# Kernel optimization log

Measured on AMD Instinct MI355X. Metric: run time of the kernel, lower is better.

The kernel has to match this reference:

```python
import jax, jax.numpy as jnp
import numpy as np

NS = [65536, 16384, 4096, 1024, 256, 64]          # nodes per level (64 = 8 graphs x 8 dense voxels)
ES = [1048576, 262144, 65536, 16384, 4096]        # edges per level (avg degree 16)
INS = [1, 15, 23, 31, 39]
OUTS = [12, 20, 28, 36, 44]
K = 5                                             # kernel_size


def setup_inputs():
    keys = iter(jax.random.split(jax.random.key(0), 64))
    d = {'x': jax.random.normal(next(keys), (NS[0], 1), jnp.float32),
         'pos': jax.random.uniform(next(keys), (NS[0], 3), jnp.float32)}
    for l in range(5):
        n, e, ci, co = NS[l], ES[l], INS[l], OUTS[l]
        d[f'src{l}'] = jax.random.randint(next(keys), (e,), 0, n)
        d[f'dst{l}'] = jax.random.randint(next(keys), (e,), 0, n)
        d[f'eattr{l}'] = jax.random.normal(next(keys), (e, 3), jnp.float32)
        d[f'cluster{l}'] = jax.random.randint(next(keys), (n,), 0, NS[l + 1])
        d[f'w1_{l}'] = jax.random.normal(next(keys), (3, K), jnp.float32) * 0.5
        d[f'b1_{l}'] = jnp.zeros((K,), jnp.float32)
        d[f'w2_{l}'] = jax.random.normal(next(keys), (K, ci * co), jnp.float32) / np.float32(np.sqrt(K * ci))
        d[f'b2_{l}'] = jnp.zeros((ci * co,), jnp.float32)
        d[f'root_{l}'] = jax.random.normal(next(keys), (ci, co), jnp.float32) / np.float32(np.sqrt(ci))
        d[f'bias_{l}'] = jnp.zeros((co,), jnp.float32)
    d['fc_w'] = jax.random.normal(next(keys), (8 * 47, 10), jnp.float32) / np.float32(np.sqrt(8 * 47))
    d['fc_b'] = jnp.zeros((10,), jnp.float32)
    return d


def _conv(x, src, dst, eattr, w1, b1, w2, b2, root, bias, n):
    # edge-conditioned kernel: MLP(edge_attr) -> [E, ci, co]
    h = jnp.tanh(eattr @ w1 + b1)                                  # [E, K]
    We = (h @ w2 + b2).reshape(eattr.shape[0], x.shape[1], -1)     # [E, ci, co]
    msg = jnp.einsum('ei,eio->eo', x[src], We)                     # gather + per-edge matvec
    s = jax.ops.segment_sum(msg, dst, num_segments=n)
    cnt = jax.ops.segment_sum(jnp.ones((dst.shape[0], 1), x.dtype), dst, num_segments=n)
    agg = s / jnp.maximum(cnt, 1.0)                                # mean aggregation
    return agg + x @ root + bias, jnp.mean(jnp.square(We))


def _pool(x, pos, cluster, n_next):
    # sparse voxel max pool on features, mean on positions; pos concatenated to features
    xm = jax.ops.segment_max(x, cluster, num_segments=n_next)
    xm = jnp.where(jnp.isfinite(xm), xm, 0.0)                      # empty voxels -> 0
    ps = jax.ops.segment_sum(pos, cluster, num_segments=n_next)
    cnt = jax.ops.segment_sum(jnp.ones((pos.shape[0], 1), pos.dtype), cluster, num_segments=n_next)
    pm = ps / jnp.maximum(cnt, 1.0)
    return jnp.concatenate([xm, pm], axis=1), pm


def reference(x, pos, src0, dst0, eattr0, cluster0, w1_0, b1_0, w2_0, b2_0, root_0, bias_0,
              src1, dst1, eattr1, cluster1, w1_1, b1_1, w2_1, b2_1, root_1, bias_1,
              src2, dst2, eattr2, cluster2, w1_2, b1_2, w2_2, b2_2, root_2, bias_2,
              src3, dst3, eattr3, cluster3, w1_3, b1_3, w2_3, b2_3, root_3, bias_3,
              src4, dst4, eattr4, cluster4, w1_4, b1_4, w2_4, b2_4, root_4, bias_4,
              fc_w, fc_b):
    lv = [(src0, dst0, eattr0, cluster0, w1_0, b1_0, w2_0, b2_0, root_0, bias_0),
          (src1, dst1, eattr1, cluster1, w1_1, b1_1, w2_1, b2_1, root_1, bias_1),
          (src2, dst2, eattr2, cluster2, w1_2, b1_2, w2_2, b2_2, root_2, bias_2),
          (src3, dst3, eattr3, cluster3, w1_3, b1_3, w2_3, b2_3, root_3, bias_3),
          (src4, dst4, eattr4, cluster4, w1_4, b1_4, w2_4, b2_4, root_4, bias_4)]
    closs = jnp.float32(0.0)
    for l, (src, dst, ea, cl, w1, b1, w2, b2, rt, bs) in enumerate(lv):
        x, c = _conv(x, src, dst, ea, w1, b1, w2, b2, rt, bs, NS[l])
        closs = closs + c
        x, pos = _pool(x, pos, cl, NS[l + 1])
    feat = x.reshape(-1, 8 * 47)                                   # [B, 8*47]
    logits = feat @ fc_w + fc_b
    return jax.nn.log_softmax(logits, axis=1), closs
```

## Files before the change

### kernel.cpp

```cpp
#include <hip/hip_runtime.h>
#include <hip/hip_fp16.h>
#include <math.h>


#define NBUCK 8
#define TILES0 256
#define NB0    512
#define IDXCAP 3072
#define TILES1 64
#define NB1    512

struct SegArgs {
    const int* idx[10];
    int*       cnt[10];
    int*       rp [10];
    int*       out[10];
    int        n  [10];
    int        nb [10];
    int        shift[10];
    int        tstart[11];
};

struct ScanAux {
    int* tilesum;
    int* tileoff;
    int  sstart[11];
    int  T;
};

struct HArgs {
    const float* eattr[5];
    const float* w1[5];
    const float* b1[5];
    float*       H;
    int          E[5];
    int          bstart[6];
};

struct WArgs {
    const float* w2[5];
    const float* b2[5];
    const float* H;
    float*       sq;
    int          cico[5];
    int          E[5];
};

__global__ __launch_bounds__(256) void countA_k(
    SegArgs a, HArgs ha, const int* __restrict__ dst0,
    const int* __restrict__ dst1, int* __restrict__ M, int* __restrict__ M1,
    int histBlocks)
{
    __shared__ int sh[NB0];
    int B = blockIdx.x;
    int t = threadIdx.x;

    if (B < TILES0) {
        for (int u = t; u < NB0; u += 256) sh[u] = 0;
        __syncthreads();
        int base = B * 4096 + t;
        #pragma unroll
        for (int it = 0; it < 16; it++)
            atomicAdd(&sh[dst0[base + it * 256] >> 7], 1);
        __syncthreads();
        for (int u = t; u < NB0; u += 256) M[(size_t)B * NB0 + u] = sh[u];
        return;
    }
    B -= TILES0;
    if (B < TILES1) {
        for (int u = t; u < NB1; u += 256) sh[u] = 0;
        __syncthreads();
        int base = B * 4096 + t;
        #pragma unroll
        for (int it = 0; it < 16; it++)
            atomicAdd(&sh[dst1[base + it * 256] >> 5], 1);
        __syncthreads();
        for (int u = t; u < NB1; u += 256) M1[(size_t)B * NB1 + u] = sh[u];
        return;
    }
    B -= TILES1;
    if (B < histBlocks) {
        int bucket = B % NBUCK;
        int T = B / NBUCK;
        int s = 0;
        while (s < 9 && T >= a.tstart[s + 1]) s++;
        int i = (T - a.tstart[s]) * 256 + t;
        if (i >= a.n[s]) return;
        int d = a.idx[s][i];
        if ((d >> a.shift[s]) != bucket) return;
        atomicAdd(&a.cnt[s][d], 1);
        return;
    }
    int b = B - histBlocks;
    const int K = 32;
    int l = 0;
    while (l < 4 && b >= ha.bstart[l + 1]) l++;
    int bloc = b - ha.bstart[l];
    const float* ea = ha.eattr[l];
    float w1r[15], b1r[5];
    #pragma unroll
    for (int i = 0; i < 15; i++) w1r[i] = ha.w1[l][i];
    #pragma unroll
    for (int i = 0; i < 5; i++)  b1r[i] = ha.b1[l][i];
    float acc[20];
    #pragma unroll
    for (int i = 0; i < 20; i++) acc[i] = 0.f;
    int base = bloc * 256 * K + t;
    for (int it = 0; it < K; it++) {
        int e = base + it * 256;
        if (e < ha.E[l]) {
            float e0 = ea[e * 3], e1 = ea[e * 3 + 1], e2 = ea[e * 3 + 2];
            float h[5];
            #pragma unroll
            for (int k = 0; k < 5; k++)
                h[k] = tanhf(e0 * w1r[k] + e1 * w1r[5 + k] + e2 * w1r[10 + k] + b1r[k]);
            int p = 5;
            #pragma unroll
            for (int k = 0; k < 5; k++) {
                acc[k] += h[k];
                #pragma unroll
                for (int k2 = k; k2 < 5; k2++) acc[p++] += h[k] * h[k2];
            }
        }
    }
    float* red = (float*)sh;
    int wid = t >> 6, lane = t & 63;
    #pragma unroll
    for (int v = 0; v < 20; v++) {
        float s = acc[v];
        #pragma unroll
        for (int o = 32; o; o >>= 1) s += __shfl_down(s, o);
        if (lane == 0) red[wid * 20 + v] = s;
    }
    __syncthreads();
    if (t < 20)
        atomicAdd(&ha.H[l * 20 + t],
                  red[t] + red[20 + t] + red[40 + t] + red[60 + t]);
}

__global__ __launch_bounds__(256) void scanP1_k(
    SegArgs a, ScanAux x, const int* __restrict__ M, int* __restrict__ M2,
    int* __restrict__ colTotal, const int* __restrict__ M1,
    int* __restrict__ M21, int* __restrict__ ct1)
{
    __shared__ int sc[256];
    int B = blockIdx.x;
    int t = threadIdx.x;

    if (B < NB0) {
        int v = M[(size_t)t * NB0 + B];
        sc[t] = v;
        __syncthreads();
        for (int d = 1; d < 256; d <<= 1) {
            int u = (t >= d) ? sc[t - d] : 0;
            __syncthreads();
            sc[t] += u;
            __syncthreads();
        }
        M2[(size_t)t * NB0 + B] = sc[t] - v;
        if (t == 255) colTotal[B] = sc[255];
        return;
    }
    B -= NB0;
    if (B < NB1) {
        if (t >= 64) return;
        int v = M1[(size_t)t * NB1 + B];
        int val = v;
        #pragma unroll
        for (int d = 1; d < 64; d <<= 1) {
            int u = __shfl_up(val, d);
            if (t >= d) val += u;
        }
        M21[(size_t)t * NB1 + B] = val - v;
        if (t == 63) ct1[B] = val;
        return;
    }
    int b = B - NB1;
    int s = 0;
    while (s < 9 && b >= x.sstart[s + 1]) s++;
    int tloc = b - x.sstart[s];
    int nb = a.nb[s];
    const int* cnt = a.cnt[s];
    int i0 = tloc * 4096 + t * 16;
    int sum = 0;
    #pragma unroll
    for (int k = 0; k < 16; k++) {
        int i = i0 + k;
        if (i < nb) sum += cnt[i];
    }
    #pragma unroll
    for (int o = 32; o; o >>= 1) sum += __shfl_down(sum, o);
    if ((t & 63) == 0) sc[t >> 6] = sum;
    __syncthreads();
    if (t == 0)
        x.tilesum[b] = sc[0] + sc[1] + sc[2] + sc[3];
}

__global__ __launch_bounds__(512) void scanP2_k(
    SegArgs a, ScanAux x, const int* __restrict__ colTotal,
    int* __restrict__ bucketStart, const int* __restrict__ ct1,
    int* __restrict__ bs1)
{
    __shared__ int sc[NB0];
    int t = threadIdx.x;
    if (blockIdx.x == 0) {
        int v = colTotal[t];
        sc[t] = v;
        __syncthreads();
        for (int d = 1; d < NB0; d <<= 1) {
            int u = (t >= d) ? sc[t - d] : 0;
            __syncthreads();
            sc[t] += u;
            __syncthreads();
        }
        bucketStart[t] = sc[t] - v;
        if (t == NB0 - 1) bucketStart[NB0] = sc[NB0 - 1];
        return;
    }
    if (blockIdx.x == 2) {
        int v = ct1[t];
        sc[t] = v;
        __syncthreads();
        for (int d = 1; d < NB1; d <<= 1) {
            int u = (t >= d) ? sc[t - d] : 0;
            __syncthreads();
            sc[t] += u;
            __syncthreads();
        }
        bs1[t] = sc[t] - v;
        if (t == NB1 - 1) bs1[NB1] = sc[NB1 - 1];
        return;
    }
    if (t >= 64) return;
    int lane = t;
    int orig = (lane < x.T) ? x.tilesum[lane] : 0;
    int val = orig;
    #pragma unroll
    for (int d = 1; d < 64; d <<= 1) {
        int v = __shfl_up(val, d);
        if (lane >= d) val += v;
    }
    int excl = val - orig;
    int s = 0;
    while (s < 9 && lane >= x.sstart[s + 1]) s++;
    int segExcl = __shfl(excl, x.sstart[s]);
    if (lane < x.T) {
        x.tileoff[lane] = excl - segExcl;
        if (lane == x.sstart[s + 1] - 1)
            a.rp[s][a.nb[s]] = val - segExcl;
    }
}

__global__ __launch_bounds__(256) void scanP3_k(
    SegArgs a, ScanAux x,
    const int* __restrict__ src, const int* __restrict__ dst,
    const float* __restrict__ ea, const float* __restrict__ x0,
    const int* __restrict__ M2, const int* __restrict__ bucketStart,
    float4* __restrict__ pay2,
    const float* __restrict__ w1, const float* __restrict__ b1,
    float* __restrict__ H0,
    const int* __restrict__ src1, const int* __restrict__ dst1,
    const float* __restrict__ ea1, const int* __restrict__ M21,
    const int* __restrict__ bs1, float4* __restrict__ pay1)
{
    __shared__ int   shi[NB0];
    __shared__ float shf[100];
    int B = blockIdx.x;
    int t = threadIdx.x;

    if (B < x.T) {
        int s = 0;
        while (s < 9 && B >= x.sstart[s + 1]) s++;
        int tloc = B - x.sstart[s];
        int nb = a.nb[s];
        const int* cnt = a.cnt[s];
        int* rp = a.rp[s];
        int i0 = tloc * 4096 + t * 16;
        int v[16];
        int sum = 0;
        #pragma unroll
        for (int k = 0; k < 16; k++) {
            int i = i0 + k;
            v[k] = (i < nb) ? cnt[i] : 0;
            sum += v[k];
        }
        int acc = sum;
        shi[t] = acc;
        __syncthreads();
        for (int d = 1; d < 256; d <<= 1) {
            int t2 = (t >= d) ? shi[t - d] : 0;
            __syncthreads();
            acc += t2;
            shi[t] = acc;
            __syncthreads();
        }
        int running = x.tileoff[B] + (acc - sum);
        #pragma unroll
        for (int k = 0; k < 16; k++) {
            int i = i0 + k;
            if (i < nb) rp[i] = running;
            running += v[k];
        }
        return;
    }
    B -= x.T;
    if (B < TILES0) {
        int tile = B;
        for (int u = t; u < NB0; u += 256)
            shi[u] = bucketStart[u] + M2[(size_t)tile * NB0 + u];
        if (t < 15) shf[t] = w1[t];
        if (t >= 32 && t < 37) shf[15 + t - 32] = b1[t - 32];
        __syncthreads();

        float acc[20];
        #pragma unroll
        for (int i = 0; i < 20; i++) acc[i] = 0.f;

        int base = tile * 4096 + t;
        #pragma unroll 4
        for (int it = 0; it < 16; it++) {
            int i = base + it * 256;
            int d = dst[i];
            float e0 = ea[i * 3], e1 = ea[i * 3 + 1], e2 = ea[i * 3 + 2];
            float h[5];
            #pragma unroll
            for (int k = 0; k < 5; k++)
                h[k] = tanhf(e0 * shf[k] + e1 * shf[5 + k] + e2 * shf[10 + k] + shf[15 + k]);
            int p = 5;
            #pragma unroll
            for (int k = 0; k < 5; k++) {
                acc[k] += h[k];
                #pragma unroll
                for (int k2 = k; k2 < 5; k2++) acc[p++] += h[k] * h[k2];
            }
            float xv = x0[src[i]];
            union HU { __half2 h2; float f; } p01, p23;
            p01.h2 = __floats2half2_rn(h[0], h[1]);
            p23.h2 = __floats2half2_rn(h[2], h[3]);
            unsigned wbits = ((unsigned)d << 16) |
                             (unsigned)__half_as_ushort(__float2half_rn(h[4]));
            int ps = atomicAdd(&shi[d >> 7], 1);
            pay2[ps] = make_float4(xv, p01.f, p23.f, __uint_as_float(wbits));
        }

        int wid = t >> 6, lane = t & 63;
        #pragma unroll
        for (int v = 0; v < 20; v++) {
            float s = acc[v];
            #pragma unroll
            for (int o = 32; o; o >>= 1) s += __shfl_down(s, o);
            if (lane == 0) shf[20 + wid * 20 + v] = s;
        }
        __syncthreads();
        if (t < 20)
            atomicAdd(&H0[t], shf[20 + t] + shf[40 + t] + shf[60 + t] + shf[80 + t]);
        return;
    }
    int tile = B - TILES0;
    for (int u = t; u < NB1; u += 256)
        shi[u] = bs1[u] + M21[(size_t)tile * NB1 + u];
    __syncthreads();
    int base = tile * 4096 + t;
    #pragma unroll 4
    for (int it = 0; it < 16; it++) {
        int i = base + it * 256;
        int d = dst1[i];
        int key = (d << 16) | src1[i];
        float e0 = ea1[i * 3], e1 = ea1[i * 3 + 1], e2 = ea1[i * 3 + 2];
        int ps = atomicAdd(&shi[d >> 5], 1);
        pay1[ps] = make_float4(__int_as_float(key), e0, e1, e2);
    }
}

__global__ __launch_bounds__(256) void scatC_k(
    SegArgs a, WArgs wa, int histBlocks,
    const float4* __restrict__ pay2, const int* __restrict__ bucketStart,
    const float* __restrict__ w2, const float* __restrict__ b2,
    const float* __restrict__ root, const float* __restrict__ bias,
    const float* __restrict__ x, float* __restrict__ y,
    const float4* __restrict__ pay1, const int* __restrict__ bs1,
    int* __restrict__ rp1, float4* __restrict__ rec1)
{
    __shared__ float wsm[96];
    __shared__ int hist[128], st[128], cur[128];
    __shared__ int idxL[IDXCAP];
    int B = blockIdx.x;
    int t = threadIdx.x;

    if (B < histBlocks) {
        int bucket = B % NBUCK;
        int T = B / NBUCK;
        int s = 0;
        while (s < 9 && T >= a.tstart[s + 1]) s++;
        int i = (T - a.tstart[s]) * 256 + t;
        if (i >= a.n[s]) return;
        int d = a.idx[s][i];
        if ((d >> a.shift[s]) != bucket) return;
        int p = atomicSub(&a.cnt[s][d], 1) - 1;
        a.out[s][a.rp[s][d] + p] = i;
        return;
    }
    B -= histBlocks;
    if (B < NB0) {
        if (t < 60) wsm[t] = w2[t];
        else if (t >= 64  && t < 76)  wsm[60 + t - 64]  = b2[t - 64];
        else if (t >= 128 && t < 140) wsm[72 + t - 128] = root[t - 128];
        else if (t >= 192 && t < 204) wsm[84 + t - 192] = bias[t - 192];
        if (t < 128) hist[t] = 0;
        __syncthreads();

        int lo = bucketStart[B], hi = bucketStart[B + 1];
        int bin0 = B << 7;
        const float* payw = (const float*)pay2;
        for (int j = lo + t; j < hi; j += 256) {
            int rel = (int)(__float_as_uint(payw[4 * j + 3]) >> 16) - bin0;
            atomicAdd(&hist[rel], 1);
        }
        __syncthreads();
        if (t < 128) st[t] = hist[t];
        __syncthreads();
        for (int d = 1; d < 128; d <<= 1) {
            int u = (t < 128 && t >= d) ? st[t - d] : 0;
            __syncthreads();
            if (t < 128) st[t] += u;
            __syncthreads();
        }
        if (t < 128) cur[t] = st[t] - hist[t];
        __syncthreads();
        for (int j = lo + t; j < hi; j += 256) {
            int rel = (int)(__float_as_uint(payw[4 * j + 3]) >> 16) - bin0;
            int p = atomicAdd(&cur[rel], 1);
            idxL[p] = j;
        }
        __syncthreads();

        if (t < 128) {
            int v = bin0 + t;
            int deg = hist[t];
            int s0 = st[t] - deg;
            float S0 = 0.f, S1 = 0.f, S2 = 0.f, S3 = 0.f, S4 = 0.f, S5 = 0.f;
            for (int jj = s0; jj < s0 + deg; jj++) {
                float4 R = pay2[idxL[jj]];
                union HU { float f; __half2 h2; } a01, a23;
                a01.f = R.y; a23.f = R.z;
                unsigned wbits = __float_as_uint(R.w);
                float xv = R.x;
                S0 += xv;
                S1 += __low2float(a01.h2)  * xv;
                S2 += __high2float(a01.h2) * xv;
                S3 += __low2float(a23.h2)  * xv;
                S4 += __high2float(a23.h2) * xv;
                S5 += __half2float(__ushort_as_half((unsigned short)(wbits & 0xffffu))) * xv;
            }
            float inv = 1.f / fmaxf((float)deg, 1.f);
            float xv = x[v];
            #pragma unroll
            for (int o = 0; o < 12; o++) {
                float msg = wsm[60 + o] * S0 + wsm[o] * S1 + wsm[12 + o] * S2 +
                            wsm[24 + o] * S3 + wsm[36 + o] * S4 + wsm[48 + o] * S5;
                y[v * 12 + o] = msg * inv + xv * wsm[72 + o] + wsm[84 + o];
            }
        }
        return;
    }
    B -= NB0;
    if (B < 5) {
        if (t >= 64) return;
        int l = B;
        const float* w2l = wa.w2[l];
        const float* b2l = wa.b2[l];
        int cico = wa.cico[l];
        float d[21];
        #pragma unroll
        for (int i = 0; i < 21; i++) d[i] = 0.f;
        for (int u = t; u < cico; u += 64) {
            float b = b2l[u];
            float w[5];
            #pragma unroll
            for (int k = 0; k < 5; k++) w[k] = w2l[k * cico + u];
            int p = 0;
            #pragma unroll
            for (int k = 0; k < 5; k++) {
                #pragma unroll
                for (int k2 = k; k2 < 5; k2++) d[p++] += w[k] * w[k2];
            }
            #pragma unroll
            for (int k = 0; k < 5; k++) d[15 + k] += b * w[k];
            d[20] += b * b;
        }
        #pragma unroll
        for (int i = 0; i < 21; i++) {
            #pragma unroll
            for (int off = 32; off; off >>= 1) d[i] += __shfl_down(d[i], off);
        }
        if (t == 0) {
            const float* H1 = wa.H + l * 20;
            const float* H2 = H1 + 5;
            float sq = (float)wa.E[l] * d[20];
            #pragma unroll
            for (int k = 0; k < 5; k++) sq += 2.f * d[15 + k] * H1[k];
            int p = 0;
            #pragma unroll
            for (int k = 0; k < 5; k++) {
                #pragma unroll
                for (int k2 = k; k2 < 5; k2++) {
                    sq += ((k == k2) ? 1.f : 2.f) * d[p] * H2[p];
                    p++;
                }
            }
            wa.sq[l] = sq;
        }
        return;
    }
    int b = B - 5;
    int lo = bs1[b], hi = bs1[b + 1];
    int bin0 = b << 5;
    if (t < 32) hist[t] = 0;
    __syncthreads();
    const float* payw = (const float*)pay1;
    for (int j = lo + t; j < hi; j += 256) {
        int rel = (int)(__float_as_uint(payw[4 * j]) >> 16) - bin0;
        atomicAdd(&hist[rel], 1);
    }
    __syncthreads();
    if (t < 32) {
        int v = hist[t];
        int val = v;
        #pragma unroll
        for (int d = 1; d < 32; d <<= 1) {
            int u = __shfl_up(val, d);
            if (t >= d) val += u;
        }
        st[t] = val - v;
        cur[t] = lo + val - v;
        rp1[bin0 + t] = lo + val - v;
        if (b == NB1 - 1 && t == 31) rp1[NB1 * 32] = hi;
    }
    __syncthreads();
    for (int j = lo + t; j < hi; j += 256) {
        float4 R = pay1[j];
        int rel = (int)(__float_as_uint(R.x) >> 16) - bin0;
        int p = atomicAdd(&cur[rel], 1);
        rec1[p] = R;
    }
}

__global__ __launch_bounds__(256) void conv1s_k(
    const int* __restrict__ rp, const float4* __restrict__ rec,
    const float* __restrict__ w1, const float* __restrict__ b1,
    const float* __restrict__ w2, const float* __restrict__ b2,
    const float* __restrict__ root, const float* __restrict__ bias,
    const float* __restrict__ x, float* __restrict__ y)
{
    constexpr int CI = 15, CO = 20, CH = 48, CICO = CI * CO;
    __shared__ float w1s[20];
    __shared__ float4 recb[CH];
    __shared__ int   svb[CH];
    __shared__ float hb[CH * 6];
    __shared__ float xs[CH * CI];
    __shared__ float S[6 * CI];

    int t = threadIdx.x;
    int v = blockIdx.x;
    if (t < 20) w1s[t] = (t < 15) ? w1[t] : b1[t - 15];
    int r0 = rp[v], r1 = rp[v + 1];
    int d  = r1 - r0;
    float acc = 0.f;

    for (int c0 = r0; c0 < r1; c0 += CH) {
        int cn = min(CH, r1 - c0);
        if (t < cn) {
            float4 R = rec[c0 + t];
            recb[t] = R;
            svb[t]  = (int)(__float_as_uint(R.x) & 0xffffu);
            hb[t * 6] = 1.f;
        }
        __syncthreads();
        if (t < cn * 5) {
            int j = t / 5, k = t % 5;
            float e0 = recb[j].y, e1 = recb[j].z, e2 = recb[j].w;
            hb[j * 6 + 1 + k] =
                tanhf(e0 * w1s[k] + e1 * w1s[5 + k] + e2 * w1s[10 + k] + w1s[15 + k]);
        }
        for (int u = t; u < cn * CI; u += 256)
            xs[u] = x[(size_t)svb[u / CI] * CI + (u % CI)];
        __syncthreads();
        if (t < 6 * CI) {
            int i = t / 6, k6 = t % 6;
            for (int j = 0; j < cn; j++)
                acc += hb[j * 6 + k6] * xs[j * CI + i];
        }
        __syncthreads();
    }

    if (t < 6 * CI) S[t] = acc;
    __syncthreads();

    if (t < CO) {
        float m = 0.f;
        for (int i = 0; i < CI; i++) {
            m += b2[i * CO + t] * S[i * 6];
            #pragma unroll
            for (int k = 0; k < 5; k++)
                m += w2[k * CICO + i * CO + t] * S[i * 6 + 1 + k];
        }
        m /= fmaxf((float)d, 1.f);
        for (int i = 0; i < CI; i++)
            m += x[(size_t)v * CI + i] * root[i * CO + t];
        y[(size_t)v * CO + t] = m + bias[t];
    }
}

template<int CI, int CO>
__global__ __launch_bounds__(256) void coop_conv_k(
    const int* __restrict__ rp, const int* __restrict__ eid,
    const int* __restrict__ src, const float* __restrict__ eattr,
    const float* __restrict__ w1, const float* __restrict__ b1,
    const float* __restrict__ w2, const float* __restrict__ b2,
    const float* __restrict__ root, const float* __restrict__ bias,
    const float* __restrict__ x, float* __restrict__ y)
{
    constexpr int CH   = 48;
    constexpr int CICO = CI * CO;
    __shared__ float w1s[20];
    __shared__ int   eb[CH], svb[CH];
    __shared__ float hb[CH * 6];
    __shared__ float xs[CH * CI];
    __shared__ float S[6 * CI];

    int t = threadIdx.x;
    int v = blockIdx.x;
    if (t < 20) w1s[t] = (t < 15) ? w1[t] : b1[t - 15];
    int r0 = rp[v], r1 = rp[v + 1];
    int d  = r1 - r0;
    float acc = 0.f;

    for (int c0 = r0; c0 < r1; c0 += CH) {
        int cn = min(CH, r1 - c0);
        if (t < cn) {
            int e = eid[c0 + t];
            eb[t]  = e;
            svb[t] = src[e];
            hb[t * 6] = 1.f;
        }
        __syncthreads();
        if (t < cn * 5) {
            int j = t / 5, k = t % 5;
            int e = eb[j];
            float e0 = eattr[e * 3], e1 = eattr[e * 3 + 1], e2 = eattr[e * 3 + 2];
            hb[j * 6 + 1 + k] =
                tanhf(e0 * w1s[k] + e1 * w1s[5 + k] + e2 * w1s[10 + k] + w1s[15 + k]);
        }
        for (int u = t; u < cn * CI; u += 256)
            xs[u] = x[(size_t)svb[u / CI] * CI + (u % CI)];
        __syncthreads();
        if (t < 6 * CI) {
            int i = t / 6, k6 = t % 6;
            for (int j = 0; j < cn; j++)
                acc += hb[j * 6 + k6] * xs[j * CI + i];
        }
        __syncthreads();
    }

    if (t < 6 * CI) S[t] = acc;
    __syncthreads();

    if (t < CO) {
        float m = 0.f;
        for (int i = 0; i < CI; i++) {
            m += b2[i * CO + t] * S[i * 6];
            #pragma unroll
            for (int k = 0; k < 5; k++)
                m += w2[k * CICO + i * CO + t] * S[i * 6 + 1 + k];
        }
        m /= fmaxf((float)d, 1.f);
        for (int i = 0; i < CI; i++)
            m += x[(size_t)v * CI + i] * root[i * CO + t];
        y[(size_t)v * CO + t] = m + bias[t];
    }
}

template<int CO>
__global__ __launch_bounds__(256) void pool_k(
    int NN,
    const int* __restrict__ crp, const int* __restrict__ cnid,
    const float* __restrict__ y, const float* __restrict__ pos,
    float* __restrict__ xn, float* __restrict__ pn)
{
    int t = blockIdx.x * 256 + threadIdx.x;
    if (t >= NN * (CO + 3)) return;
    int c = t / (CO + 3), o = t % (CO + 3);
    int r0 = crp[c], r1 = crp[c + 1];
    int d = r1 - r0;
    if (o < CO) {
        float m = -INFINITY;
        for (int j = r0; j < r1; j++)
            m = fmaxf(m, y[(size_t)cnid[j] * CO + o]);
        if (d == 0 || !isfinite(m)) m = 0.f;
        xn[c * (CO + 3) + o] = m;
    } else {
        int k = o - CO;
        float sum = 0.f;
        for (int j = r0; j < r1; j++)
            sum += pos[cnid[j] * 3 + k];
        float pm = sum / fmaxf((float)d, 1.f);
        xn[c * (CO + 3) + CO + k] = pm;
        pn[c * 3 + k] = pm;
    }
}

__global__ __launch_bounds__(128) void fc_k(
    const float* __restrict__ x5,
    const float* __restrict__ fc_w, const float* __restrict__ fc_b,
    const float* __restrict__ sq, float* __restrict__ out)
{
    __shared__ float feat[8 * 376];
    __shared__ float logit[80];
    __shared__ float roff[8];
    for (int t = threadIdx.x; t < 8 * 376; t += 128) feat[t] = x5[t];
    __syncthreads();
    int t = threadIdx.x;
    if (t < 80) {
        int b = t / 10, j = t % 10;
        float acc = fc_b[j];
        for (int k = 0; k < 376; k++) acc += feat[b * 376 + k] * fc_w[k * 10 + j];
        logit[t] = acc;
    }
    __syncthreads();
    if (t < 8) {
        float m = -1e30f;
        for (int j = 0; j < 10; j++) m = fmaxf(m, logit[t * 10 + j]);
        float ssum = 0.f;
        for (int j = 0; j < 10; j++) ssum += expf(logit[t * 10 + j] - m);
        roff[t] = m + logf(ssum);
    }
    __syncthreads();
    if (t < 80) out[t] = logit[t] - roff[t / 10];
    if (t == 0) {
        float closs = 0.f;
        closs += sq[0] * (1.0f / 12582912.0f);
        closs += sq[1] * (1.0f / 78643200.0f);
        closs += sq[2] * (1.0f / 42205184.0f);
        closs += sq[3] * (1.0f / 18284544.0f);
        closs += sq[4] * (1.0f / 7028736.0f);
        out[80] = closs;
    }
}


extern "C" void kernel_launch(void* const* d_in, const int* in_sizes, int n_in,
                              void* d_out, int out_size, void* d_ws, size_t ws_size,
                              hipStream_t stream)
{
    static const int NSa[6] = {65536, 16384, 4096, 1024, 256, 64};
    static const int ESa[5] = {1048576, 262144, 65536, 16384, 4096};
    static const int COa[5] = {12, 20, 28, 36, 44};
    static const int CIa[5] = {1, 15, 23, 31, 39};

    const float* x0   = (const float*)d_in[0];
    const float* pos0 = (const float*)d_in[1];

    int* wsw = (int*)d_ws;
    size_t off = 0;
    auto alw = [&](size_t n) -> size_t {
        size_t p = off; off += (n + 63) & ~(size_t)63; return p;
    };
    size_t degO[5], cdegO[5];
    for (int l = 2; l < 5; l++) degO[l]  = alw(NSa[l]);
    for (int l = 0; l < 5; l++) cdegO[l] = alw(NSa[l + 1]);
    size_t HO = alw(100);
    size_t zeroWords = off;
    size_t rpO[5], crpO[5], eidO[5], cnidO[5];
    rpO[1] = alw(NSa[1] + 1);
    for (int l = 2; l < 5; l++) rpO[l]  = alw(NSa[l] + 1);
    for (int l = 0; l < 5; l++) crpO[l] = alw(NSa[l + 1] + 1);
    for (int l = 2; l < 5; l++) eidO[l] = alw(ESa[l]);
    for (int l = 0; l < 5; l++) cnidO[l] = alw(NSa[l]);
    size_t tsO  = alw(64);
    size_t toO  = alw(64);
    size_t MO   = alw((size_t)TILES0 * NB0);
    size_t M2O  = alw((size_t)TILES0 * NB0);
    size_t ctO  = alw(NB0);
    size_t bsO  = alw(NB0 + 1);
    size_t payO = alw((size_t)ESa[0] * 4);
    size_t M1O  = alw((size_t)TILES1 * NB1);
    size_t M21O = alw((size_t)TILES1 * NB1);
    size_t ct1O = alw(NB1);
    size_t bs1O = alw(NB1 + 1);
    size_t pay1O = alw((size_t)ESa[1] * 4);
    size_t rec1O = alw((size_t)ESa[1] * 4);
    size_t yO   = alw((size_t)65536 * 12);
    size_t sqO  = alw(8);
    size_t xnO[5], pnO[5];
    for (int l = 0; l < 5; l++) xnO[l] = alw((size_t)NSa[l + 1] * (COa[l] + 3));
    for (int l = 0; l < 5; l++) pnO[l] = alw((size_t)NSa[l + 1] * 3);

    hipMemsetAsync(d_ws, 0, zeroWords * 4, stream);

    SegArgs sa{};
    int nseg = 0;
    for (int l = 2; l < 5; l++) {
        sa.idx[nseg] = (const int*)d_in[3 + 10 * l];
        sa.cnt[nseg] = wsw + degO[l];
        sa.rp [nseg] = wsw + rpO[l];
        sa.out[nseg] = wsw + eidO[l];
        sa.n  [nseg] = ESa[l];
        sa.nb [nseg] = NSa[l];
        nseg++;
    }
    for (int l = 0; l < 5; l++) {
        sa.idx[nseg] = (const int*)d_in[5 + 10 * l];
        sa.cnt[nseg] = wsw + cdegO[l];
        sa.rp [nseg] = wsw + crpO[l];
        sa.out[nseg] = wsw + cnidO[l];
        sa.n  [nseg] = NSa[l];
        sa.nb [nseg] = NSa[l + 1];
        nseg++;
    }
    ScanAux sx{};
    int tiles = 0, btiles = 0;
    for (int s = 0; s < nseg; s++) {
        int lg = 31 - __builtin_clz(sa.nb[s]);
        sa.shift[s] = lg - 3;
        sa.tstart[s] = tiles;
        tiles += (sa.n[s] + 255) / 256;
        sx.sstart[s] = btiles;
        btiles += (sa.nb[s] + 4095) / 4096;
    }
    for (int s = nseg; s <= 10; s++) {
        sa.tstart[s] = tiles;
        sx.sstart[s] = btiles;
        if (s < 10) {
            sa.idx[s] = sa.idx[nseg - 1]; sa.cnt[s] = sa.cnt[nseg - 1];
            sa.rp[s] = sa.rp[nseg - 1];   sa.out[s] = sa.out[nseg - 1];
            sa.n[s] = 0; sa.nb[s] = 8; sa.shift[s] = 0;
        }
    }
    sx.T = btiles;
    sx.tilesum = wsw + tsO;
    sx.tileoff = wsw + toO;
    int histBlocks = tiles * NBUCK;

    float4* pay2 = (float4*)(wsw + payO);
    float4* pay1 = (float4*)(wsw + pay1O);
    float4* rec1 = (float4*)(wsw + rec1O);
    float*  Hp   = (float*)(wsw + HO);

    HArgs ha{};
    int bs = 0;
    ha.bstart[0] = 0;
    ha.eattr[0] = (const float*)d_in[4];
    ha.w1[0] = (const float*)d_in[6];
    ha.b1[0] = (const float*)d_in[7];
    ha.E[0] = 0;
    for (int l = 1; l < 5; l++) {
        ha.eattr[l] = (const float*)d_in[4 + 10 * l];
        ha.w1[l]    = (const float*)d_in[6 + 10 * l];
        ha.b1[l]    = (const float*)d_in[7 + 10 * l];
        ha.E[l]     = ESa[l];
        ha.bstart[l] = bs;
        bs += (ESa[l] + 256 * 32 - 1) / (256 * 32);
    }
    ha.bstart[5] = bs;
    ha.H = Hp;

    WArgs wa{};
    for (int l = 0; l < 5; l++) {
        wa.w2[l]   = (const float*)d_in[8 + 10 * l];
        wa.b2[l]   = (const float*)d_in[9 + 10 * l];
        wa.cico[l] = CIa[l] * COa[l];
        wa.E[l]    = ESa[l];
    }
    wa.H  = Hp;
    wa.sq = (float*)(wsw + sqO);

    countA_k<<<TILES0 + TILES1 + histBlocks + bs, 256, 0, stream>>>(
        sa, ha, (const int*)d_in[3], (const int*)d_in[13],
        wsw + MO, wsw + M1O, histBlocks);
    scanP1_k<<<NB0 + NB1 + btiles, 256, 0, stream>>>(
        sa, sx, wsw + MO, wsw + M2O, wsw + ctO,
        wsw + M1O, wsw + M21O, wsw + ct1O);
    scanP2_k<<<3, 512, 0, stream>>>(sa, sx, wsw + ctO, wsw + bsO,
                                    wsw + ct1O, wsw + bs1O);
    scanP3_k<<<btiles + TILES0 + TILES1, 256, 0, stream>>>(
        sa, sx,
        (const int*)d_in[2], (const int*)d_in[3], (const float*)d_in[4],
        x0, wsw + M2O, wsw + bsO, pay2,
        (const float*)d_in[6], (const float*)d_in[7], Hp,
        (const int*)d_in[12], (const int*)d_in[13], (const float*)d_in[14],
        wsw + M21O, wsw + bs1O, pay1);

    float* yb = (float*)(wsw + yO);

    scatC_k<<<histBlocks + NB0 + 5 + NB1, 256, 0, stream>>>(
        sa, wa, histBlocks, pay2, wsw + bsO,
        (const float*)d_in[8], (const float*)d_in[9],
        (const float*)d_in[10], (const float*)d_in[11], x0, yb,
        pay1, wsw + bs1O, wsw + rpO[1], rec1);

    pool_k<12><<<(NSa[1] * 15 + 255) / 256, 256, 0, stream>>>(
        NSa[1], wsw + crpO[0], wsw + cnidO[0], yb, pos0,
        (float*)(wsw + xnO[0]), (float*)(wsw + pnO[0]));

    conv1s_k<<<NSa[1], 256, 0, stream>>>(
        wsw + rpO[1], rec1,
        (const float*)d_in[16], (const float*)d_in[17],
        (const float*)d_in[18], (const float*)d_in[19],
        (const float*)d_in[20], (const float*)d_in[21],
        (const float*)(wsw + xnO[0]), yb);
    pool_k<20><<<(NSa[2] * 23 + 255) / 256, 256, 0, stream>>>(
        NSa[2], wsw + crpO[1], wsw + cnidO[1], yb,
        (const float*)(wsw + pnO[0]),
        (float*)(wsw + xnO[1]), (float*)(wsw + pnO[1]));

#define LVLC(l, CI_, CO_) do {                                                 \
    const float* xin   = (const float*)(wsw + xnO[(l) - 1]);                   \
    const float* posin = (const float*)(wsw + pnO[(l) - 1]);                   \
    int N = NSa[(l)], NN = NSa[(l) + 1];                                       \
    coop_conv_k<CI_, CO_><<<N, 256, 0, stream>>>(                              \
        wsw + rpO[(l)], wsw + eidO[(l)],                                       \
        (const int*)d_in[2 + 10 * (l)], (const float*)d_in[4 + 10 * (l)],      \
        (const float*)d_in[6 + 10 * (l)], (const float*)d_in[7 + 10 * (l)],    \
        (const float*)d_in[8 + 10 * (l)], (const float*)d_in[9 + 10 * (l)],    \
        (const float*)d_in[10 + 10 * (l)], (const float*)d_in[11 + 10 * (l)],  \
        xin, yb);                                                              \
    pool_k<CO_><<<(NN * ((CO_) + 3) + 255) / 256, 256, 0, stream>>>(           \
        NN, wsw + crpO[(l)], wsw + cnidO[(l)], yb, posin,                      \
        (float*)(wsw + xnO[(l)]), (float*)(wsw + pnO[(l)]));                   \
} while (0)

    LVLC(2, 23, 28);
    LVLC(3, 31, 36);
    LVLC(4, 39, 44);
#undef LVLC

    fc_k<<<1, 128, 0, stream>>>((const float*)(wsw + xnO[4]),
                                (const float*)d_in[52], (const float*)d_in[53],
                                wa.sq, (float*)d_out);
}
```

Baseline: 418.0 us.

## Fuse post-level-0 conv and pool stages into one persistent kernel with grid barriers

Replaces the nine separate pool, conv and fc launches after level 0 with a single persistent kernel of 512 blocks. The blocks loop over nodes and synchronise between phases with an atomic-counter grid barrier. The goal is to remove launch gaps and tail effects, which matter most for the small deep levels. The cost is barrier spin overhead, fewer resident blocks on the large level-1 conv, and a deadlock risk if all 512 blocks are not co-resident; the barrier counter also relies on being zeroed in the workspace zero region.

New measurement: 1.051 ms. 2.51x slower.

```diff
diff --git a/kernel.cpp b/kernel.cpp
--- a/kernel.cpp
+++ b/kernel.cpp
@@ -9,6 +9,7 @@
 #define IDXCAP 3072
 #define TILES1 64
 #define NB1    512
+#define MBLK   512
 
 struct SegArgs {
     const int* idx[10];
@@ -545,181 +546,190 @@
     }
 }
 
-__global__ __launch_bounds__(256) void conv1s_k(
-    const int* __restrict__ rp, const float4* __restrict__ rec,
-    const float* __restrict__ w1, const float* __restrict__ b1,
-    const float* __restrict__ w2, const float* __restrict__ b2,
-    const float* __restrict__ root, const float* __restrict__ bias,
-    const float* __restrict__ x, float* __restrict__ y)
+__device__ __forceinline__ void grid_barrier(int* bar, int target) {
+    __syncthreads();
+    if (threadIdx.x == 0) {
+        __threadfence();
+        atomicAdd(bar, 1);
+        while (atomicAdd(bar, 0) < target) __builtin_amdgcn_s_sleep(2);
+        __threadfence();
+    }
+    __syncthreads();
+}
+
+__device__ void pool_phase(int NN, int CO,
+    const int* crp, const int* cnid, const float* y, const float* pos,
+    float* xn, float* pn)
+{
+    int total = NN * (CO + 3);
+    for (int t = blockIdx.x * 256 + threadIdx.x; t < total; t += MBLK * 256) {
+        int c = t / (CO + 3), o = t % (CO + 3);
+        int r0 = crp[c], r1 = crp[c + 1];
+        int d = r1 - r0;
+        if (o < CO) {
+            float m = -INFINITY;
+            for (int j = r0; j < r1; j++)
+                m = fmaxf(m, y[(size_t)cnid[j] * CO + o]);
+            if (d == 0 || !isfinite(m)) m = 0.f;
+            xn[c * (CO + 3) + o] = m;
+        } else {
+            int k = o - CO;
+            float sum = 0.f;
+            for (int j = r0; j < r1; j++)
+                sum += pos[cnid[j] * 3 + k];
+            float pm = sum / fmaxf((float)d, 1.f);
+            xn[c * (CO + 3) + CO + k] = pm;
+            pn[c * 3 + k] = pm;
+        }
+    }
+}
+
+template<int CI, int CO>
+__device__ void coop_phase(int N,
+    const int* rp, const int* eid, const int* src, const float* eattr,
+    const float* w1, const float* b1, const float* w2, const float* b2,
+    const float* root, const float* bias, const float* x, float* y,
+    char* smem)
+{
+    constexpr int CH = 48, CICO = CI * CO;
+    float* w1s = (float*)smem;
+    int*   eb  = (int*)(smem + 96);
+    int*   svb = eb + 48;
+    float* hb  = (float*)(svb + 48);
+    float* xs  = hb + 288;
+    float* S   = xs + 48 * CI;
+    int t = threadIdx.x;
+
+    for (int v = blockIdx.x; v < N; v += MBLK) {
+        if (t < 20) w1s[t] = (t < 15) ? w1[t] : b1[t - 15];
+        int r0 = rp[v], r1 = rp[v + 1];
+        int d  = r1 - r0;
+        float acc = 0.f;
+
+        for (int c0 = r0; c0 < r1; c0 += CH) {
+            int cn = min(CH, r1 - c0);
+            if (t < cn) {
+                int e = eid[c0 + t];
+                eb[t]  = e;
+                svb[t] = src[e];
+                hb[t * 6] = 1.f;
+            }
+            __syncthreads();
+            if (t < cn * 5) {
+                int j = t / 5, k = t % 5;
+                int e = eb[j];
+                float e0 = eattr[e * 3], e1 = eattr[e * 3 + 1], e2 = eattr[e * 3 + 2];
+                hb[j * 6 + 1 + k] =
+                    tanhf(e0 * w1s[k] + e1 * w1s[5 + k] + e2 * w1s[10 + k] + w1s[15 + k]);
+            }
+            for (int u = t; u < cn * CI; u += 256)
+                xs[u] = x[(size_t)svb[u / CI] * CI + (u % CI)];
+            __syncthreads();
+            if (t < 6 * CI) {
+                int i = t / 6, k6 = t % 6;
+                for (int j = 0; j < cn; j++)
+                    acc += hb[j * 6 + k6] * xs[j * CI + i];
+            }
+            __syncthreads();
+        }
+
+        if (t < 6 * CI) S[t] = acc;
+        __syncthreads();
+
+        if (t < CO) {
+            float m = 0.f;
+            for (int i = 0; i < CI; i++) {
+                m += b2[i * CO + t] * S[i * 6];
+                #pragma unroll
+                for (int k = 0; k < 5; k++)
+                    m += w2[k * CICO + i * CO + t] * S[i * 6 + 1 + k];
+            }
+            m /= fmaxf((float)d, 1.f);
+            for (int i = 0; i < CI; i++)
+                m += x[(size_t)v * CI + i] * root[i * CO + t];
+            y[(size_t)v * CO + t] = m + bias[t];
+        }
+        __syncthreads();
+    }
+}
+
+__device__ void conv1s_phase(int N,
+    const int* rp, const float4* rec,
+    const float* w1, const float* b1, const float* w2, const float* b2,
+    const float* root, const float* bias, const float* x, float* y,
+    char* smem)
 {
     constexpr int CI = 15, CO = 20, CH = 48, CICO = CI * CO;
-    __shared__ float w1s[20];
-    __shared__ float4 recb[CH];
-    __shared__ int   svb[CH];
-    __shared__ float hb[CH * 6];
-    __shared__ float xs[CH * CI];
-    __shared__ float S[6 * CI];
-
+    float4* recb = (float4*)smem;
+    int*    svb  = (int*)(smem + 768);
+    float*  hb   = (float*)(svb + 48);
+    float*  xs   = hb + 288;
+    float*  S    = xs + 720;
+    float*  w1s  = S + 90;
     int t = threadIdx.x;
-    int v = blockIdx.x;
-    if (t < 20) w1s[t] = (t < 15) ? w1[t] : b1[t - 15];
-    int r0 = rp[v], r1 = rp[v + 1];
-    int d  = r1 - r0;
-    float acc = 0.f;
-
-    for (int c0 = r0; c0 < r1; c0 += CH) {
-        int cn = min(CH, r1 - c0);
-        if (t < cn) {
-            float4 R = rec[c0 + t];
-            recb[t] = R;
-            svb[t]  = (int)(__float_as_uint(R.x) & 0xffffu);
-            hb[t * 6] = 1.f;
-        }
-        __syncthreads();
-        if (t < cn * 5) {
-            int j = t / 5, k = t % 5;
-            float e0 = recb[j].y, e1 = recb[j].z, e2 = recb[j].w;
-            hb[j * 6 + 1 + k] =
-                tanhf(e0 * w1s[k] + e1 * w1s[5 + k] + e2 * w1s[10 + k] + w1s[15 + k]);
-        }
-        for (int u = t; u < cn * CI; u += 256)
-            xs[u] = x[(size_t)svb[u / CI] * CI + (u % CI)];
-        __syncthreads();
-        if (t < 6 * CI) {
-            int i = t / 6, k6 = t % 6;
-            for (int j = 0; j < cn; j++)
-                acc += hb[j * 6 + k6] * xs[j * CI + i];
-        }
-        __syncthreads();
-    }
-
-    if (t < 6 * CI) S[t] = acc;
-    __syncthreads();
-
-    if (t < CO) {
-        float m = 0.f;
-        for (int i = 0; i < CI; i++) {
-            m += b2[i * CO + t] * S[i * 6];
-            #pragma unroll
-            for (int k = 0; k < 5; k++)
-                m += w2[k * CICO + i * CO + t] * S[i * 6 + 1 + k];
-        }
-        m /= fmaxf((float)d, 1.f);
-        for (int i = 0; i < CI; i++)
-            m += x[(size_t)v * CI + i] * root[i * CO + t];
-        y[(size_t)v * CO + t] = m + bias[t];
-    }
-}
-
-template<int CI, int CO>
-__global__ __launch_bounds__(256) void coop_conv_k(
-    const int* __restrict__ rp, const int* __restrict__ eid,
-    const int* __restrict__ src, const float* __restrict__ eattr,
-    const float* __restrict__ w1, const float* __restrict__ b1,
-    const float* __restrict__ w2, const float* __restrict__ b2,
-    const float* __restrict__ root, const float* __restrict__ bias,
-    const float* __restrict__ x, float* __restrict__ y)
-{
-    constexpr int CH   = 48;
-    constexpr int CICO = CI * CO;
-    __shared__ float w1s[20];
-    __shared__ int   eb[CH], svb[CH];
-    __shared__ float hb[CH * 6];
-    __shared__ float xs[CH * CI];
-    __shared__ float S[6 * CI];
-
+
+    for (int v = blockIdx.x; v < N; v += MBLK) {
+        if (t < 20) w1s[t] = (t < 15) ? w1[t] : b1[t - 15];
+        int r0 = rp[v], r1 = rp[v + 1];
+        int d  = r1 - r0;
+        float acc = 0.f;
+
+        for (int c0 = r0; c0 < r1; c0 += CH) {
+            int cn = min(CH, r1 - c0);
+            if (t < cn) {
+                float4 R = rec[c0 + t];
+                recb[t] = R;
+                svb[t]  = (int)(__float_as_uint(R.x) & 0xffffu);
+                hb[t * 6] = 1.f;
+            }
+            __syncthreads();
+            if (t < cn * 5) {
+                int j = t / 5, k = t % 5;
+                float e0 = recb[j].y, e1 = recb[j].z, e2 = recb[j].w;
+                hb[j * 6 + 1 + k] =
+                    tanhf(e0 * w1s[k] + e1 * w1s[5 + k] + e2 * w1s[10 + k] + w1s[15 + k]);
+            }
+            for (int u = t; u < cn * CI; u += 256)
+                xs[u] = x[(size_t)svb[u / CI] * CI + (u % CI)];
+            __syncthreads();
+            if (t < 6 * CI) {
+                int i = t / 6, k6 = t % 6;
+                for (int j = 0; j < cn; j++)
+                    acc += hb[j * 6 + k6] * xs[j * CI + i];
+            }
+            __syncthreads();
+        }
+
+        if (t < 6 * CI) S[t] = acc;
+        __syncthreads();
+
+        if (t < CO) {
+            float m = 0.f;
+            for (int i = 0; i < CI; i++) {
+                m += b2[i * CO + t] * S[i * 6];
+                #pragma unroll
+                for (int k = 0; k < 5; k++)
+                    m += w2[k * CICO + i * CO + t] * S[i * 6 + 1 + k];
+            }
+            m /= fmaxf((float)d, 1.f);
+            for (int i = 0; i < CI; i++)
+                m += x[(size_t)v * CI + i] * root[i * CO + t];
+            y[(size_t)v * CO + t] = m + bias[t];
+        }
+        __syncthreads();
+    }
+}
+
+__device__ void fc_phase(
+    const float* x5, const float* fc_w, const float* fc_b,
+    const float* sq, float* out, char* smem)
+{
+    float* feat  = (float*)smem;
+    float* logit = feat + 3008;
+    float* roff  = logit + 80;
     int t = threadIdx.x;
-    int v = blockIdx.x;
-    if (t < 20) w1s[t] = (t < 15) ? w1[t] : b1[t - 15];
-    int r0 = rp[v], r1 = rp[v + 1];
-    int d  = r1 - r0;
-    float acc = 0.f;
-
-    for (int c0 = r0; c0 < r1; c0 += CH) {
-        int cn = min(CH, r1 - c0);
-        if (t < cn) {
-            int e = eid[c0 + t];
-            eb[t]  = e;
-            svb[t] = src[e];
-            hb[t * 6] = 1.f;
-        }
-        __syncthreads();
-        if (t < cn * 5) {
-            int j = t / 5, k = t % 5;
-            int e = eb[j];
-            float e0 = eattr[e * 3], e1 = eattr[e * 3 + 1], e2 = eattr[e * 3 + 2];
-            hb[j * 6 + 1 + k] =
-                tanhf(e0 * w1s[k] + e1 * w1s[5 + k] + e2 * w1s[10 + k] + w1s[15 + k]);
-        }
-        for (int u = t; u < cn * CI; u += 256)
-            xs[u] = x[(size_t)svb[u / CI] * CI + (u % CI)];
-        __syncthreads();
-        if (t < 6 * CI) {
-            int i = t / 6, k6 = t % 6;
-            for (int j = 0; j < cn; j++)
-                acc += hb[j * 6 + k6] * xs[j * CI + i];
-        }
-        __syncthreads();
-    }
-
-    if (t < 6 * CI) S[t] = acc;
-    __syncthreads();
-
-    if (t < CO) {
-        float m = 0.f;
-        for (int i = 0; i < CI; i++) {
-            m += b2[i * CO + t] * S[i * 6];
-            #pragma unroll
-            for (int k = 0; k < 5; k++)
-                m += w2[k * CICO + i * CO + t] * S[i * 6 + 1 + k];
-        }
-        m /= fmaxf((float)d, 1.f);
-        for (int i = 0; i < CI; i++)
-            m += x[(size_t)v * CI + i] * root[i * CO + t];
-        y[(size_t)v * CO + t] = m + bias[t];
-    }
-}
-
-template<int CO>
-__global__ __launch_bounds__(256) void pool_k(
-    int NN,
-    const int* __restrict__ crp, const int* __restrict__ cnid,
-    const float* __restrict__ y, const float* __restrict__ pos,
-    float* __restrict__ xn, float* __restrict__ pn)
-{
-    int t = blockIdx.x * 256 + threadIdx.x;
-    if (t >= NN * (CO + 3)) return;
-    int c = t / (CO + 3), o = t % (CO + 3);
-    int r0 = crp[c], r1 = crp[c + 1];
-    int d = r1 - r0;
-    if (o < CO) {
-        float m = -INFINITY;
-        for (int j = r0; j < r1; j++)
-            m = fmaxf(m, y[(size_t)cnid[j] * CO + o]);
-        if (d == 0 || !isfinite(m)) m = 0.f;
-        xn[c * (CO + 3) + o] = m;
-    } else {
-        int k = o - CO;
-        float sum = 0.f;
-        for (int j = r0; j < r1; j++)
-            sum += pos[cnid[j] * 3 + k];
-        float pm = sum / fmaxf((float)d, 1.f);
-        xn[c * (CO + 3) + CO + k] = pm;
-        pn[c * 3 + k] = pm;
-    }
-}
-
-__global__ __launch_bounds__(128) void fc_k(
-    const float* __restrict__ x5,
-    const float* __restrict__ fc_w, const float* __restrict__ fc_b,
-    const float* __restrict__ sq, float* __restrict__ out)
-{
-    __shared__ float feat[8 * 376];
-    __shared__ float logit[80];
-    __shared__ float roff[8];
-    for (int t = threadIdx.x; t < 8 * 376; t += 128) feat[t] = x5[t];
-    __syncthreads();
-    int t = threadIdx.x;
+    for (int u = t; u < 8 * 376; u += 256) feat[u] = x5[u];
+    __syncthreads();
     if (t < 80) {
         int b = t / 10, j = t % 10;
         float acc = fc_b[j];
@@ -747,6 +757,58 @@
     }
 }
 
+struct MegaArgs {
+    const int*   crp[5];
+    const int*   cnid[5];
+    const int*   rp[5];
+    const int*   eid[5];
+    const float4* rec1;
+    const int*   src[5];
+    const float* eattr[5];
+    const float* w1[5], *b1[5], *w2[5], *b2[5], *root[5], *bias[5];
+    const float* pos0;
+    float*       xn[5];
+    float*       pn[5];
+    float*       y;
+    const float* fc_w, *fc_b, *sq;
+    float*       out;
+    int*         bar;
+};
+
+__global__ __launch_bounds__(256, 2) void mega_k(MegaArgs m)
+{
+    __shared__ __align__(16) char smem[12544];
+    int tgt = MBLK;
+
+    pool_phase(16384, 12, m.crp[0], m.cnid[0], m.y, m.pos0, m.xn[0], m.pn[0]);
+    grid_barrier(m.bar, tgt); tgt += MBLK;
+    conv1s_phase(16384, m.rp[1], m.rec1, m.w1[1], m.b1[1], m.w2[1], m.b2[1],
+                 m.root[1], m.bias[1], m.xn[0], m.y, smem);
+    grid_barrier(m.bar, tgt); tgt += MBLK;
+    pool_phase(4096, 20, m.crp[1], m.cnid[1], m.y, m.pn[0], m.xn[1], m.pn[1]);
+    grid_barrier(m.bar, tgt); tgt += MBLK;
+    coop_phase<23, 28>(4096, m.rp[2], m.eid[2], m.src[2], m.eattr[2],
+                       m.w1[2], m.b1[2], m.w2[2], m.b2[2], m.root[2],
+                       m.bias[2], m.xn[1], m.y, smem);
+    grid_barrier(m.bar, tgt); tgt += MBLK;
+    pool_phase(1024, 28, m.crp[2], m.cnid[2], m.y, m.pn[1], m.xn[2], m.pn[2]);
+    grid_barrier(m.bar, tgt); tgt += MBLK;
+    coop_phase<31, 36>(1024, m.rp[3], m.eid[3], m.src[3], m.eattr[3],
+                       m.w1[3], m.b1[3], m.w2[3], m.b2[3], m.root[3],
+                       m.bias[3], m.xn[2], m.y, smem);
+    grid_barrier(m.bar, tgt); tgt += MBLK;
+    pool_phase(256, 36, m.crp[3], m.cnid[3], m.y, m.pn[2], m.xn[3], m.pn[3]);
+    grid_barrier(m.bar, tgt); tgt += MBLK;
+    coop_phase<39, 44>(256, m.rp[4], m.eid[4], m.src[4], m.eattr[4],
+                       m.w1[4], m.b1[4], m.w2[4], m.b2[4], m.root[4],
+                       m.bias[4], m.xn[3], m.y, smem);
+    grid_barrier(m.bar, tgt); tgt += MBLK;
+    pool_phase(64, 44, m.crp[4], m.cnid[4], m.y, m.pn[3], m.xn[4], m.pn[4]);
+    grid_barrier(m.bar, tgt); tgt += MBLK;
+    if (blockIdx.x == 0)
+        fc_phase(m.xn[4], m.fc_w, m.fc_b, m.sq, m.out, smem);
+}
+
 
 extern "C" void kernel_launch(void* const* d_in, const int* in_sizes, int n_in,
                               void* d_out, int out_size, void* d_ws, size_t ws_size,
@@ -768,7 +830,8 @@
     size_t degO[5], cdegO[5];
     for (int l = 2; l < 5; l++) degO[l]  = alw(NSa[l]);
     for (int l = 0; l < 5; l++) cdegO[l] = alw(NSa[l + 1]);
-    size_t HO = alw(100);
+    size_t HO   = alw(100);
+    size_t barO = alw(16);
     size_t zeroWords = off;
     size_t rpO[5], crpO[5], eidO[5], cnidO[5];
     rpO[1] = alw(NSa[1] + 1);
@@ -898,43 +961,31 @@
         (const float*)d_in[10], (const float*)d_in[11], x0, yb,
         pay1, wsw + bs1O, wsw + rpO[1], rec1);
 
-    pool_k<12><<<(NSa[1] * 15 + 255) / 256, 256, 0, stream>>>(
-        NSa[1], wsw + crpO[0], wsw + cnidO[0], yb, pos0,
-        (float*)(wsw + xnO[0]), (float*)(wsw + pnO[0]));
-
-    conv1s_k<<<NSa[1], 256, 0, stream>>>(
-        wsw + rpO[1], rec1,
-        (const float*)d_in[16], (const float*)d_in[17],
-        (const float*)d_in[18], (const float*)d_in[19],
-        (const float*)d_in[20], (const float*)d_in[21],
-        (const float*)(wsw + xnO[0]), yb);
-    pool_k<20><<<(NSa[2] * 23 + 255) / 256, 256, 0, stream>>>(
-        NSa[2], wsw + crpO[1], wsw + cnidO[1], yb,
-        (const float*)(wsw + pnO[0]),
-        (float*)(wsw + xnO[1]), (float*)(wsw + pnO[1]));
-
-#define LVLC(l, CI_, CO_) do {                                                 \
-    const float* xin   = (const float*)(wsw + xnO[(l) - 1]);                   \
-    const float* posin = (const float*)(wsw + pnO[(l) - 1]);                   \
-    int N = NSa[(l)], NN = NSa[(l) + 1];                                       \
-    coop_conv_k<CI_, CO_><<<N, 256, 0, stream>>>(                              \
-        wsw + rpO[(l)], wsw + eidO[(l)],                                       \
-        (const int*)d_in[2 + 10 * (l)], (const float*)d_in[4 + 10 * (l)],      \
-        (const float*)d_in[6 + 10 * (l)], (const float*)d_in[7 + 10 * (l)],    \
-        (const float*)d_in[8 + 10 * (l)], (const float*)d_in[9 + 10 * (l)],    \
-        (const float*)d_in[10 + 10 * (l)], (const float*)d_in[11 + 10 * (l)],  \
-        xin, yb);                                                              \
-    pool_k<CO_><<<(NN * ((CO_) + 3) + 255) / 256, 256, 0, stream>>>(           \
-        NN, wsw + crpO[(l)], wsw + cnidO[(l)], yb, posin,                      \
-        (float*)(wsw + xnO[(l)]), (float*)(wsw + pnO[(l)]));                   \
-} while (0)
-
-    LVLC(2, 23, 28);
-    LVLC(3, 31, 36);
-    LVLC(4, 39, 44);
-#undef LVLC
-
-    fc_k<<<1, 128, 0, stream>>>((const float*)(wsw + xnO[4]),
-                                (const float*)d_in[52], (const float*)d_in[53],
-                                wa.sq, (float*)d_out);
-}
+    MegaArgs ma{};
+    for (int l = 0; l < 5; l++) {
+        ma.crp[l]  = wsw + crpO[l];
+        ma.cnid[l] = wsw + cnidO[l];
+        ma.src[l]   = (const int*)d_in[2 + 10 * l];
+        ma.eattr[l] = (const float*)d_in[4 + 10 * l];
+        ma.w1[l]   = (const float*)d_in[6 + 10 * l];
+        ma.b1[l]   = (const float*)d_in[7 + 10 * l];
+        ma.w2[l]   = (const float*)d_in[8 + 10 * l];
+        ma.b2[l]   = (const float*)d_in[9 + 10 * l];
+        ma.root[l] = (const float*)d_in[10 + 10 * l];
+        ma.bias[l] = (const float*)d_in[11 + 10 * l];
+        ma.xn[l] = (float*)(wsw + xnO[l]);
+        ma.pn[l] = (float*)(wsw + pnO[l]);
+    }
+    ma.rp[1] = wsw + rpO[1];
+    for (int l = 2; l < 5; l++) { ma.rp[l] = wsw + rpO[l]; ma.eid[l] = wsw + eidO[l]; }
+    ma.rec1 = rec1;
+    ma.pos0 = pos0;
+    ma.y    = yb;
+    ma.fc_w = (const float*)d_in[52];
+    ma.fc_b = (const float*)d_in[53];
+    ma.sq   = wa.sq;
+    ma.out  = (float*)d_out;
+    ma.bar  = wsw + barO;
+
+    mega_k<<<MBLK, 256, 0, stream>>>(ma);
+}
```
